# Optimization experiments

Hardware: AMD Instinct MI355X
Metric: run time of the kernel (lower is better)

Reference implementation:

```python
import jax, jax.numpy as jnp
import numpy as np

NUM_EMBEDDINGS = 1024
EMBEDDING_DIM = 64
COMMIT_COST = 0.25


def setup_inputs() -> dict:
    key = jax.random.key(0)
    k1, k2 = jax.random.split(key)
    latent = jax.random.normal(k1, (32, EMBEDDING_DIM, 32, 32), dtype=jnp.float32)
    embedding_weight = jax.random.normal(k2, (NUM_EMBEDDINGS, EMBEDDING_DIM), dtype=jnp.float32)
    return {"latent": latent, "embedding_weight": embedding_weight}


def reference(latent, embedding_weight):
    # rearrange 'b n j d -> b j d n'; n == embedding_dim
    lat = jnp.transpose(latent, (0, 2, 3, 1))  # [b, j, d, n]
    flat = lat.reshape(-1, EMBEDDING_DIM)      # [T, D]
    # squared-euclidean distances [T, K]
    distances = (
        jnp.sum(flat ** 2, axis=1, keepdims=True)
        + jnp.sum(embedding_weight ** 2, axis=1)
        - 2.0 * flat @ embedding_weight.T
    )
    idx = jnp.argmin(distances, axis=1)                         # [T]
    encodings = jax.nn.one_hot(idx, NUM_EMBEDDINGS, dtype=flat.dtype)  # [T, K]
    quantized_flat = embedding_weight[idx]                      # gather == encodings @ W
    quantized = quantized_flat.reshape(lat.shape)               # [b, j, d, n]

    e_latent_loss = jnp.mean((jax.lax.stop_gradient(quantized) - lat) ** 2)
    loss = COMMIT_COST * e_latent_loss

    # straight-through estimator
    quantized_st = lat + jax.lax.stop_gradient(quantized - lat)

    avg_probs = jnp.mean(encodings, axis=0)
    perplexity = jnp.exp(-jnp.sum(avg_probs * jnp.log(avg_probs + 1e-10)))

    # rearrange back 'b j d n -> b n j d'
    quantized_out = jnp.transpose(quantized_st, (0, 3, 1, 2))
    return quantized_out, loss, perplexity, encodings, distances
```

## Files before the change

### kernel.cpp

```cpp
#include <hip/hip_runtime.h>
#include <cfloat>

#define T_TOTAL 32768
#define DIM 64
#define KCODES 1024

static constexpr long long OFF_Q    = 0;
static constexpr long long OFF_LOSS = 2097152;
static constexpr long long OFF_PERP = 2097153;
static constexpr long long OFF_ENC  = 2097154;
static constexpr long long OFF_DIST = 2097154LL + 33554432LL;


__global__ __launch_bounds__(256) void vq_prep_kernel(const float* __restrict__ W,
                                                      float* __restrict__ ww,
                                                      float* __restrict__ WT) {
    const int tid = threadIdx.x;
    if (blockIdx.x < 256) {
        const int lane = tid & 63;
        const int code = blockIdx.x * 4 + (tid >> 6);
        float v = W[code * DIM + lane];
        float s = v * v;
        #pragma unroll
        for (int off = 32; off > 0; off >>= 1)
            s += __shfl_down(s, off, 64);
        if (lane == 0) ww[code] = s;
    } else {
        const int n = blockIdx.x - 256;
        #pragma unroll
        for (int i = 0; i < 4; ++i) {
            int k = i * 256 + tid;
            WT[n * KCODES + k] = W[k * DIM + n];
        }
    }
}

__global__ __launch_bounds__(256, 3) void vq_main_kernel(const float* __restrict__ lat,
                                                         const float* __restrict__ W,
                                                         const float* __restrict__ ww,
                                                         const float* __restrict__ WT,
                                                         float* __restrict__ out,
                                                         int* __restrict__ counts,
                                                         float* __restrict__ lossSum) {
    __shared__ float xT[64 * 64];
    __shared__ float wS[32 * 256];
    __shared__ float xx[64];
    __shared__ int   selIdx[64];

    const int tid = threadIdx.x;
    const int tx  = tid & 31;
    const int ty  = tid >> 5;
    const int t0  = blockIdx.x * 64;
    const long long base = (long long)(t0 >> 10) * 65536 + (long long)(t0 & 1023);

    #pragma unroll
    for (int i = 0; i < 16; ++i) {
        int e  = i * 256 + tid;
        int n  = e >> 6;
        int tl = e & 63;
        xT[n * 64 + tl] = lat[base + (long long)n * 1024 + tl];
    }
    __syncthreads();
    if (tid < 64) {
        float s = 0.f;
        #pragma unroll 8
        for (int n = 0; n < 64; ++n) {
            float v = xT[n * 64 + tid];
            s = fmaf(v, v, s);
        }
        xx[tid] = s;
    }

    float minV[8];
    int   minI[8];
    #pragma unroll
    for (int r = 0; r < 8; ++r) { minV[r] = FLT_MAX; minI[r] = 0; }

    float* __restrict__ distOut = out + OFF_DIST;

    for (int c = 0; c < 4; ++c) {
        float acc[8][8];
        #pragma unroll
        for (int r = 0; r < 8; ++r)
            #pragma unroll
            for (int k = 0; k < 8; ++k) acc[r][k] = 0.f;

        for (int h = 0; h < 2; ++h) {
            __syncthreads();
            #pragma unroll
            for (int i = 0; i < 8; ++i) {
                int e2 = i * 256 + tid;
                int n  = e2 >> 6;
                int k4 = e2 & 63;
                *(float4*)&wS[n * 256 + k4 * 4] =
                    *(const float4*)&WT[(h * 32 + n) * KCODES + c * 256 + k4 * 4];
            }
            __syncthreads();

            #pragma unroll 4
            for (int nn = 0; nn < 32; ++nn) {
                const float* xrow = &xT[(h * 32 + nn) * 64];
                const float* wrow = &wS[nn * 256];
                float4 a0 = *(const float4*)&xrow[ty * 4];
                float4 a1 = *(const float4*)&xrow[32 + ty * 4];
                float4 b0 = *(const float4*)&wrow[tx * 4];
                float4 b1 = *(const float4*)&wrow[128 + tx * 4];
                float ar[8] = {a0.x, a0.y, a0.z, a0.w, a1.x, a1.y, a1.z, a1.w};
                float br[8] = {b0.x, b0.y, b0.z, b0.w, b1.x, b1.y, b1.z, b1.w};
                #pragma unroll
                for (int r = 0; r < 8; ++r)
                    #pragma unroll
                    for (int k = 0; k < 8; ++k)
                        acc[r][k] = fmaf(ar[r], br[k], acc[r][k]);
            }
        }

        const int kb0 = c * 256 + tx * 4;
        float wr[8];
        #pragma unroll
        for (int k = 0; k < 8; ++k)
            wr[k] = ww[kb0 + (k >> 2) * 128 + (k & 3)];
        #pragma unroll
        for (int r = 0; r < 8; ++r) {
            const int row = (r >> 2) * 32 + ty * 4 + (r & 3);
            const float xxr = xx[row];
            float d[8];
            #pragma unroll
            for (int k = 0; k < 8; ++k) {
                d[k] = (xxr + wr[k]) - 2.f * acc[r][k];
                int ki = kb0 + (k >> 2) * 128 + (k & 3);
                if (d[k] < minV[r]) { minV[r] = d[k]; minI[r] = ki; }
            }
            const long long ro = (long long)(t0 + row) * KCODES + kb0;
            *(float2*)&distOut[ro]           = make_float2(d[0], d[1]);
            *(float2*)&distOut[ro + 2]       = make_float2(d[2], d[3]);
            *(float2*)&distOut[ro + 128]     = make_float2(d[4], d[5]);
            *(float2*)&distOut[ro + 130]     = make_float2(d[6], d[7]);
        }
    }

    __syncthreads();
    float* redV = wS;
    int*   redI = (int*)(wS + 64 * 33);
    #pragma unroll
    for (int r = 0; r < 8; ++r) {
        const int row = (r >> 2) * 32 + ty * 4 + (r & 3);
        redV[row * 33 + tx] = minV[r];
        redI[row * 33 + tx] = minI[r];
    }
    __syncthreads();
    if (tid < 64) {
        float best = redV[tid * 33];
        int   bi   = redI[tid * 33];
        #pragma unroll
        for (int s = 1; s < 32; ++s) {
            float v  = redV[tid * 33 + s];
            int   i2 = redI[tid * 33 + s];
            if (v < best || (v == best && i2 < bi)) { best = v; bi = i2; }
        }
        selIdx[tid] = bi;
        atomicAdd(&counts[bi], 1);
    }
    __syncthreads();

    float* qS = wS;
    #pragma unroll
    for (int i = 0; i < 16; ++i) {
        int e   = i * 256 + tid;
        int row = e >> 6;
        int n   = e & 63;
        qS[row * 65 + n] = W[selIdx[row] * DIM + n];
    }
    __syncthreads();

    float ls = 0.f;
    #pragma unroll
    for (int i = 0; i < 4; ++i) {
        int e2  = i * 256 + tid;
        int n   = e2 >> 4;
        int tl0 = (e2 & 15) * 4;
        float q0 = qS[(tl0 + 0) * 65 + n];
        float q1 = qS[(tl0 + 1) * 65 + n];
        float q2 = qS[(tl0 + 2) * 65 + n];
        float q3 = qS[(tl0 + 3) * 65 + n];
        float x0 = xT[n * 64 + tl0 + 0];
        float x1 = xT[n * 64 + tl0 + 1];
        float x2 = xT[n * 64 + tl0 + 2];
        float x3 = xT[n * 64 + tl0 + 3];
        *(float4*)&out[OFF_Q + base + (long long)n * 1024 + tl0] = make_float4(q0, q1, q2, q3);
        float e0 = q0 - x0; ls = fmaf(e0, e0, ls);
        float e1 = q1 - x1; ls = fmaf(e1, e1, ls);
        float e2d = q2 - x2; ls = fmaf(e2d, e2d, ls);
        float e3 = q3 - x3; ls = fmaf(e3, e3, ls);
    }
    #pragma unroll
    for (int off = 32; off > 0; off >>= 1)
        ls += __shfl_down(ls, off, 64);
    if ((tid & 63) == 0) atomicAdd(lossSum, ls);

    float* __restrict__ enc = out + OFF_ENC;
    for (int i = 0; i < 128; ++i) {
        int e2  = i * 256 + tid;
        int row = e2 >> 9;
        int k2  = (e2 & 511) * 2;
        int sel = selIdx[row];
        float2 v;
        v.x = (k2     == sel) ? 1.f : 0.f;
        v.y = (k2 + 1 == sel) ? 1.f : 0.f;
        *(float2*)&enc[(long long)(t0 + row) * KCODES + k2] = v;
    }
}

__global__ __launch_bounds__(1024) void vq_finalize_kernel(const int* __restrict__ counts,
                                                           const float* __restrict__ lossSum,
                                                           float* __restrict__ out) {
    __shared__ float red[16];
    const int tid = threadIdx.x;
    float p = (float)counts[tid] * (1.0f / 32768.0f);
    float term = p * logf(p + 1e-10f);
    #pragma unroll
    for (int off = 32; off > 0; off >>= 1)
        term += __shfl_down(term, off, 64);
    if ((tid & 63) == 0) red[tid >> 6] = term;
    __syncthreads();
    if (tid == 0) {
        float s = 0.f;
        #pragma unroll
        for (int i = 0; i < 16; ++i) s += red[i];
        out[OFF_PERP] = expf(-s);
        out[OFF_LOSS] = 0.25f * lossSum[0] * (1.0f / 2097152.0f);
    }
}

extern "C" void kernel_launch(void* const* d_in, const int* in_sizes, int n_in,
                              void* d_out, int out_size, void* d_ws, size_t ws_size,
                              hipStream_t stream) {
    (void)in_sizes; (void)n_in; (void)out_size; (void)ws_size;
    const float* lat = (const float*)d_in[0];
    const float* W   = (const float*)d_in[1];
    float* out = (float*)d_out;

    int*   counts  = (int*)d_ws;
    float* ww      = (float*)((char*)d_ws + 4096);
    float* lossSum = (float*)((char*)d_ws + 8192);
    float* WT      = (float*)((char*)d_ws + 12288);

    hipMemsetAsync(d_ws, 0, 8192 + 16, stream);

    vq_prep_kernel<<<320, 256, 0, stream>>>(W, ww, WT);
    vq_main_kernel<<<512, 256, 0, stream>>>(lat, W, ww, WT, out, counts, lossSum);
    vq_finalize_kernel<<<1, 1024, 0, stream>>>(counts, lossSum, out);
}
```

Baseline: 340.2 us.

## Split VQ into distance and epilogue kernels with one code per thread

Replaces the tiled shared-memory GEMM kernel with three stages. The prep kernel transposes the latent into token-major scratch (stored in the encodings output region) and computes the per-token squared norms. A distance kernel then holds one code's weights in registers per thread, computes each token's distance, writes it with a nontemporal store and finds the argmin with wave shuffles and a ballot. Partial minima go to the quantized output region, and an epilogue kernel reduces them, gathers the selected codes, and writes the loss and one-hot encodings with nontemporal stores. This raises parallelism, but each per-row loop is a scalar dot product that reads the token row from global memory, and staging scratch data in the output buffers adds extra global traffic.

```diff
diff --git a/kernel.cpp b/kernel.cpp
--- a/kernel.cpp
+++ b/kernel.cpp
@@ -4,6 +4,8 @@
 #define T_TOTAL 32768
 #define DIM 64
 #define KCODES 1024
+
+typedef float f32x2 __attribute__((ext_vector_type(2)));
 
 static constexpr long long OFF_Q    = 0;
 static constexpr long long OFF_LOSS = 2097152;
@@ -11,10 +13,14 @@
 static constexpr long long OFF_ENC  = 2097154;
 static constexpr long long OFF_DIST = 2097154LL + 33554432LL;
 
+static constexpr long long OFF_XTG = OFF_ENC;
+static constexpr long long OFF_XX  = OFF_ENC + 2097152LL;
+
 
 __global__ __launch_bounds__(256) void vq_prep_kernel(const float* __restrict__ W,
+                                                      const float* __restrict__ lat,
                                                       float* __restrict__ ww,
-                                                      float* __restrict__ WT) {
+                                                      float* __restrict__ out) {
     const int tid = threadIdx.x;
     if (blockIdx.x < 256) {
         const int lane = tid & 63;
@@ -25,34 +31,125 @@
         for (int off = 32; off > 0; off >>= 1)
             s += __shfl_down(s, off, 64);
         if (lane == 0) ww[code] = s;
-    } else {
-        const int n = blockIdx.x - 256;
-        #pragma unroll
-        for (int i = 0; i < 4; ++i) {
-            int k = i * 256 + tid;
-            WT[n * KCODES + k] = W[k * DIM + n];
-        }
-    }
-}
-
-__global__ __launch_bounds__(256, 3) void vq_main_kernel(const float* __restrict__ lat,
-                                                         const float* __restrict__ W,
+        return;
+    }
+    __shared__ float tile[256 * 17];
+    const int bi  = blockIdx.x - 256;
+    const int b   = bi >> 2;
+    const int jd0 = (bi & 3) * 256;
+    float* __restrict__ xTg = out + OFF_XTG;
+    float* __restrict__ xxg = out + OFF_XX;
+    float sp = 0.f;
+    for (int g = 0; g < 4; ++g) {
+        if (g) __syncthreads();
+        #pragma unroll
+        for (int it = 0; it < 16; ++it) {
+            float v = lat[(long long)b * 65536 + (g * 16 + it) * 1024 + jd0 + tid];
+            tile[tid * 17 + it] = v;
+            sp = fmaf(v, v, sp);
+        }
+        __syncthreads();
+        #pragma unroll
+        for (int it = 0; it < 16; ++it) {
+            int rl = it * 16 + (tid >> 4);
+            int n  = tid & 15;
+            xTg[(long long)(b * 1024 + jd0 + rl) * 64 + g * 16 + n] = tile[rl * 17 + n];
+        }
+    }
+    xxg[b * 1024 + jd0 + tid] = sp;
+}
+
+__global__ __launch_bounds__(256, 4) void vq_dist_kernel(const float* __restrict__ W,
                                                          const float* __restrict__ ww,
-                                                         const float* __restrict__ WT,
-                                                         float* __restrict__ out,
-                                                         int* __restrict__ counts,
-                                                         float* __restrict__ lossSum) {
+                                                         float* __restrict__ out) {
+    __shared__ float pv[64 * 4];
+    __shared__ int   pi[64 * 4];
+
+    const int tid  = threadIdx.x;
+    const int lane = tid & 63;
+    const int w    = tid >> 6;
+    const int s    = blockIdx.x & 3;
+    const int rowBase = (blockIdx.x >> 2) * 64;
+    const int code = s * 256 + w * 64 + lane;
+
+    float4 bb[16];
+    const float4* wp4 = (const float4*)(W + code * DIM);
+    #pragma unroll
+    for (int i = 0; i < 16; ++i) bb[i] = wp4[i];
+    const float wwv = ww[code];
+
+    const float* __restrict__ xTg = out + OFF_XTG;
+    const float* __restrict__ xxg = out + OFF_XX;
+    float* __restrict__ dist = out + OFF_DIST;
+
+    for (int r = 0; r < 64; ++r) {
+        const int row = rowBase + r;
+        const float* xr = xTg + (long long)row * 64;
+        float acc = 0.f;
+        #pragma unroll
+        for (int i = 0; i < 16; ++i) {
+            acc = fmaf(xr[i * 4 + 0], bb[i].x, acc);
+            acc = fmaf(xr[i * 4 + 1], bb[i].y, acc);
+            acc = fmaf(xr[i * 4 + 2], bb[i].z, acc);
+            acc = fmaf(xr[i * 4 + 3], bb[i].w, acc);
+        }
+        const float d = (xxg[row] + wwv) - 2.f * acc;
+        float m = d;
+        #pragma unroll
+        for (int off = 1; off < 64; off <<= 1)
+            m = fminf(m, __shfl_xor(m, off, 64));
+        unsigned long long msk = __ballot(d == m);
+        if (lane == 0) {
+            int ml = (int)__builtin_ctzll(msk);
+            pv[r * 4 + w] = m;
+            pi[r * 4 + w] = s * 256 + w * 64 + ml;
+        }
+        __builtin_nontemporal_store(d, &dist[(long long)row * KCODES + code]);
+    }
+    __syncthreads();
+
+    if (tid < 64) {
+        float best = pv[tid * 4];
+        int   bi   = pi[tid * 4];
+        #pragma unroll
+        for (int q = 1; q < 4; ++q) {
+            float v  = pv[tid * 4 + q];
+            int   i2 = pi[tid * 4 + q];
+            if (v < best || (v == best && i2 < bi)) { best = v; bi = i2; }
+        }
+        const int row = rowBase + tid;
+        const long long qb = (long long)(row >> 10) * 65536 + (row & 1023);
+        out[OFF_Q + qb + (long long)(s * 2)     * 1024] = best;
+        out[OFF_Q + qb + (long long)(s * 2 + 1) * 1024] = __int_as_float(bi);
+    }
+}
+
+__global__ __launch_bounds__(256) void vq_epi_kernel(const float* __restrict__ lat,
+                                                     const float* __restrict__ W,
+                                                     float* __restrict__ out,
+                                                     int* __restrict__ counts,
+                                                     float* __restrict__ lossSum) {
     __shared__ float xT[64 * 64];
-    __shared__ float wS[32 * 256];
-    __shared__ float xx[64];
-    __shared__ int   selIdx[64];
+    __shared__ float qS[64 * 65];
+    __shared__ int   selS[64];
 
     const int tid = threadIdx.x;
-    const int tx  = tid & 31;
-    const int ty  = tid >> 5;
     const int t0  = blockIdx.x * 64;
     const long long base = (long long)(t0 >> 10) * 65536 + (long long)(t0 & 1023);
 
+    if (tid < 64) {
+        const long long qb = base + tid;
+        float best = out[OFF_Q + qb];
+        int   bi   = __float_as_int(out[OFF_Q + qb + 1024]);
+        #pragma unroll
+        for (int s = 1; s < 4; ++s) {
+            float v  = out[OFF_Q + qb + (long long)(s * 2) * 1024];
+            int   i2 = __float_as_int(out[OFF_Q + qb + (long long)(s * 2 + 1) * 1024]);
+            if (v < best || (v == best && i2 < bi)) { best = v; bi = i2; }
+        }
+        selS[tid] = bi;
+        atomicAdd(&counts[bi], 1);
+    }
     #pragma unroll
     for (int i = 0; i < 16; ++i) {
         int e  = i * 256 + tid;
@@ -61,115 +158,13 @@
         xT[n * 64 + tl] = lat[base + (long long)n * 1024 + tl];
     }
     __syncthreads();
-    if (tid < 64) {
-        float s = 0.f;
-        #pragma unroll 8
-        for (int n = 0; n < 64; ++n) {
-            float v = xT[n * 64 + tid];
-            s = fmaf(v, v, s);
-        }
-        xx[tid] = s;
-    }
-
-    float minV[8];
-    int   minI[8];
-    #pragma unroll
-    for (int r = 0; r < 8; ++r) { minV[r] = FLT_MAX; minI[r] = 0; }
-
-    float* __restrict__ distOut = out + OFF_DIST;
-
-    for (int c = 0; c < 4; ++c) {
-        float acc[8][8];
-        #pragma unroll
-        for (int r = 0; r < 8; ++r)
-            #pragma unroll
-            for (int k = 0; k < 8; ++k) acc[r][k] = 0.f;
-
-        for (int h = 0; h < 2; ++h) {
-            __syncthreads();
-            #pragma unroll
-            for (int i = 0; i < 8; ++i) {
-                int e2 = i * 256 + tid;
-                int n  = e2 >> 6;
-                int k4 = e2 & 63;
-                *(float4*)&wS[n * 256 + k4 * 4] =
-                    *(const float4*)&WT[(h * 32 + n) * KCODES + c * 256 + k4 * 4];
-            }
-            __syncthreads();
-
-            #pragma unroll 4
-            for (int nn = 0; nn < 32; ++nn) {
-                const float* xrow = &xT[(h * 32 + nn) * 64];
-                const float* wrow = &wS[nn * 256];
-                float4 a0 = *(const float4*)&xrow[ty * 4];
-                float4 a1 = *(const float4*)&xrow[32 + ty * 4];
-                float4 b0 = *(const float4*)&wrow[tx * 4];
-                float4 b1 = *(const float4*)&wrow[128 + tx * 4];
-                float ar[8] = {a0.x, a0.y, a0.z, a0.w, a1.x, a1.y, a1.z, a1.w};
-                float br[8] = {b0.x, b0.y, b0.z, b0.w, b1.x, b1.y, b1.z, b1.w};
-                #pragma unroll
-                for (int r = 0; r < 8; ++r)
-                    #pragma unroll
-                    for (int k = 0; k < 8; ++k)
-                        acc[r][k] = fmaf(ar[r], br[k], acc[r][k]);
-            }
-        }
-
-        const int kb0 = c * 256 + tx * 4;
-        float wr[8];
-        #pragma unroll
-        for (int k = 0; k < 8; ++k)
-            wr[k] = ww[kb0 + (k >> 2) * 128 + (k & 3)];
-        #pragma unroll
-        for (int r = 0; r < 8; ++r) {
-            const int row = (r >> 2) * 32 + ty * 4 + (r & 3);
-            const float xxr = xx[row];
-            float d[8];
-            #pragma unroll
-            for (int k = 0; k < 8; ++k) {
-                d[k] = (xxr + wr[k]) - 2.f * acc[r][k];
-                int ki = kb0 + (k >> 2) * 128 + (k & 3);
-                if (d[k] < minV[r]) { minV[r] = d[k]; minI[r] = ki; }
-            }
-            const long long ro = (long long)(t0 + row) * KCODES + kb0;
-            *(float2*)&distOut[ro]           = make_float2(d[0], d[1]);
-            *(float2*)&distOut[ro + 2]       = make_float2(d[2], d[3]);
-            *(float2*)&distOut[ro + 128]     = make_float2(d[4], d[5]);
-            *(float2*)&distOut[ro + 130]     = make_float2(d[6], d[7]);
-        }
-    }
-
-    __syncthreads();
-    float* redV = wS;
-    int*   redI = (int*)(wS + 64 * 33);
-    #pragma unroll
-    for (int r = 0; r < 8; ++r) {
-        const int row = (r >> 2) * 32 + ty * 4 + (r & 3);
-        redV[row * 33 + tx] = minV[r];
-        redI[row * 33 + tx] = minI[r];
-    }
-    __syncthreads();
-    if (tid < 64) {
-        float best = redV[tid * 33];
-        int   bi   = redI[tid * 33];
-        #pragma unroll
-        for (int s = 1; s < 32; ++s) {
-            float v  = redV[tid * 33 + s];
-            int   i2 = redI[tid * 33 + s];
-            if (v < best || (v == best && i2 < bi)) { best = v; bi = i2; }
-        }
-        selIdx[tid] = bi;
-        atomicAdd(&counts[bi], 1);
-    }
-    __syncthreads();
-
-    float* qS = wS;
+
     #pragma unroll
     for (int i = 0; i < 16; ++i) {
         int e   = i * 256 + tid;
         int row = e >> 6;
         int n   = e & 63;
-        qS[row * 65 + n] = W[selIdx[row] * DIM + n];
+        qS[row * 65 + n] = W[selS[row] * DIM + n];
     }
     __syncthreads();
 
@@ -199,15 +194,16 @@
     if ((tid & 63) == 0) atomicAdd(lossSum, ls);
 
     float* __restrict__ enc = out + OFF_ENC;
+    #pragma unroll 4
     for (int i = 0; i < 128; ++i) {
         int e2  = i * 256 + tid;
         int row = e2 >> 9;
         int k2  = (e2 & 511) * 2;
-        int sel = selIdx[row];
-        float2 v;
+        int sel = selS[row];
+        f32x2 v;
         v.x = (k2     == sel) ? 1.f : 0.f;
         v.y = (k2 + 1 == sel) ? 1.f : 0.f;
-        *(float2*)&enc[(long long)(t0 + row) * KCODES + k2] = v;
+        __builtin_nontemporal_store(v, (f32x2*)&enc[(long long)(t0 + row) * KCODES + k2]);
     }
 }
 
@@ -243,11 +239,11 @@
     int*   counts  = (int*)d_ws;
     float* ww      = (float*)((char*)d_ws + 4096);
     float* lossSum = (float*)((char*)d_ws + 8192);
-    float* WT      = (float*)((char*)d_ws + 12288);
-
-    hipMemsetAsync(d_ws, 0, 8192 + 16, stream);
-
-    vq_prep_kernel<<<320, 256, 0, stream>>>(W, ww, WT);
-    vq_main_kernel<<<512, 256, 0, stream>>>(lat, W, ww, WT, out, counts, lossSum);
+
+    (void)hipMemsetAsync(d_ws, 0, 8192 + 16, stream);
+
+    vq_prep_kernel<<<384, 256, 0, stream>>>(W, lat, ww, out);
+    vq_dist_kernel<<<2048, 256, 0, stream>>>(W, ww, out);
+    vq_epi_kernel<<<512, 256, 0, stream>>>(lat, W, out, counts, lossSum);
     vq_finalize_kernel<<<1, 1024, 0, stream>>>(counts, lossSum, out);
 }
```

Result: slower. 581.9 us (+71.0%).
